# Kernel tuning notes

Measured on AMD Instinct MI355X. Metric: run time of the kernel, lower is better.

Reference implementation:

```python
import jax, jax.numpy as jnp
import numpy as np

B, S, D, H, L, F = 16, 256, 512, 1024, 2, 2048  # batch, seq, inner, head(clusters), layers, ffnn
HID = D // 2
LN_EPS = 1e-5


def _lstm_dir(x, Wih, Whh, bih, bhh, reverse=False):
    # x: [B,S,D] -> hs: [B,S,HID]; PyTorch gate order i,f,g,o
    if reverse:
        x = x[:, ::-1]
    xT = jnp.swapaxes(x, 0, 1)                    # [S,B,D]
    pre = xT @ Wih.T + (bih + bhh)                # precompute input contribution [S,B,4*HID]
    z = jnp.zeros((x.shape[0], Whh.shape[1]), x.dtype)

    def step(carry, p):
        h, c = carry
        g = p + h @ Whh.T
        i, f, gg, o = jnp.split(g, 4, axis=-1)
        c = jax.nn.sigmoid(f) * c + jax.nn.sigmoid(i) * jnp.tanh(gg)
        h = jax.nn.sigmoid(o) * jnp.tanh(c)
        return (h, c), h

    _, hs = jax.lax.scan(step, (z, z), pre)
    hs = jnp.swapaxes(hs, 0, 1)                   # [B,S,HID]
    if reverse:
        hs = hs[:, ::-1]
    return hs


def _layernorm(x, g, b):
    mu = jnp.mean(x, axis=-1, keepdims=True)
    var = jnp.mean(jnp.square(x - mu), axis=-1, keepdims=True)
    return (x - mu) * jax.lax.rsqrt(var + LN_EPS) * g + b


def _forward(input_sequence, label_embeddings, out_proj,
             Wih_f, Whh_f, bih_f, bhh_f, Wih_b, Whh_b, bih_b, bhh_b,
             ffnn_w1, ffnn_b1, ffnn_w2, ffnn_b2, ln_g, ln_b):
    fwd = _lstm_dir(input_sequence, Wih_f, Whh_f, bih_f, bhh_f, reverse=False)
    bwd = _lstm_dir(input_sequence, Wih_b, Whh_b, bih_b, bhh_b, reverse=True)
    features = jnp.concatenate([fwd, bwd], axis=-1)          # [B,S,D]

    query = jnp.broadcast_to(label_embeddings, (input_sequence.shape[0], H, D))
    for l in range(L):
        # self-attention (no scaling, as in source)
        w = jax.nn.softmax(jnp.einsum('bqd,bkd->bqk', query, query), axis=-1)
        q1 = jnp.einsum('bqk,bkd->bqd', w, query)
        # cross-attention onto LSTM features
        w2 = jax.nn.softmax(jnp.einsum('bqd,bsd->bqs', q1, features), axis=-1)
        q2 = jnp.einsum('bqs,bsd->bqd', w2, features)
        # FFN + LayerNorm
        h = jax.nn.gelu(q2 @ ffnn_w1[l] + ffnn_b1[l], approximate=False) @ ffnn_w2[l] + ffnn_b2[l]
        query = _layernorm(h, ln_g[l], ln_b[l])
    # (query @ output) * eye @ ones  ==  diagonal of the matmul == batched dot
    return jnp.einsum('bhd,dh->bh', query, out_proj)


def setup_inputs() -> dict:
    ks = jax.random.split(jax.random.key(0), 20)
    s_lstm = 1.0 / np.sqrt(HID)
    s_ff = 0.02
    clusters = jax.random.normal(ks[0], (H, D), jnp.float32) * s_ff
    return {
        'input_sequence': jax.random.normal(ks[1], (B, S, D), jnp.float32),
        'label_embeddings': clusters,
        'out_proj': clusters.T,
        'Wih_f': jax.random.normal(ks[2], (4 * HID, D), jnp.float32) * s_lstm,
        'Whh_f': jax.random.normal(ks[3], (4 * HID, HID), jnp.float32) * s_lstm,
        'bih_f': jax.random.normal(ks[4], (4 * HID,), jnp.float32) * s_lstm,
        'bhh_f': jax.random.normal(ks[5], (4 * HID,), jnp.float32) * s_lstm,
        'Wih_b': jax.random.normal(ks[6], (4 * HID, D), jnp.float32) * s_lstm,
        'Whh_b': jax.random.normal(ks[7], (4 * HID, HID), jnp.float32) * s_lstm,
        'bih_b': jax.random.normal(ks[8], (4 * HID,), jnp.float32) * s_lstm,
        'bhh_b': jax.random.normal(ks[9], (4 * HID,), jnp.float32) * s_lstm,
        'ffnn_w1': jax.random.normal(ks[10], (L, D, F), jnp.float32) * s_ff,
        'ffnn_b1': jnp.zeros((L, F), jnp.float32),
        'ffnn_w2': jax.random.normal(ks[11], (L, F, D), jnp.float32) * s_ff,
        'ffnn_b2': jnp.zeros((L, D), jnp.float32),
        'ln_g': jnp.ones((L, D), jnp.float32),
        'ln_b': jnp.zeros((L, D), jnp.float32),
    }


def reference(input_sequence, label_embeddings, out_proj,
              Wih_f, Whh_f, bih_f, bhh_f, Wih_b, Whh_b, bih_b, bhh_b,
              ffnn_w1, ffnn_b1, ffnn_w2, ffnn_b2, ln_g, ln_b):
    return _forward(input_sequence, label_embeddings, out_proj,
                    Wih_f, Whh_f, bih_f, bhh_f, Wih_b, Whh_b, bih_b, bhh_b,
                    ffnn_w1, ffnn_b1, ffnn_w2, ffnn_b2, ln_g, ln_b)
```

## Files before the change

kernel.cpp:

```cpp
#include <hip/hip_runtime.h>
#include <hip/hip_bf16.h>
#include <math.h>

#define NB 16
#define NS 256
#define ND 512
#define NH 1024
#define NF 2048
#define NHID 256

typedef __attribute__((ext_vector_type(8))) short bf16x8;
typedef __attribute__((ext_vector_type(4))) float f32x4;

__device__ __forceinline__ unsigned short f2bf(float f) {
    unsigned u = __float_as_uint(f);
    unsigned r = u + 0x7fffu + ((u >> 16) & 1u);
    return (unsigned short)(r >> 16);
}
__device__ __forceinline__ float bf2f(unsigned short h) {
    return __uint_as_float(((unsigned)h) << 16);
}
__device__ __forceinline__ float sigmoid_fast(float x) {
    return 1.0f / (1.0f + __expf(-x));
}
__device__ __forceinline__ float tanh_fast(float x) {
    return 1.0f - 2.0f / (__expf(2.0f * x) + 1.0f);
}

template<int PASSES, int ACT, int OUT>
__global__ __launch_bounds__(256) void sgemm4(
    const unsigned short* __restrict__ Ahi, const unsigned short* __restrict__ Alo,
    const unsigned short* __restrict__ Bhi, const unsigned short* __restrict__ Blo,
    const float* __restrict__ bias,
    float* __restrict__ C, unsigned short* __restrict__ Chi, unsigned short* __restrict__ Clo,
    int M, int N, int K, int lda, int ldb, long sA, long sB, long sC)
{
    __shared__ unsigned short Ah[128 * 32];
    __shared__ unsigned short Bh[128 * 32];
    __shared__ unsigned short Al[(PASSES == 3) ? 128 * 32 : 64];
    __shared__ unsigned short Bl[(PASSES == 3) ? 128 * 32 : 64];

    const int t = threadIdx.x;
    const int z = blockIdx.z;
    const int m0 = blockIdx.y * 128, n0 = blockIdx.x * 128;
    const int wid = t >> 6, lane = t & 63;
    const int wr = (wid >> 1) * 64, wc = (wid & 1) * 64;
    const int lr = lane & 15, lk = lane >> 4;
    const int rl = lane >> 2, sl = lane & 3;

    const unsigned short* pAh = Ahi + (size_t)z * sA;
    const unsigned short* pBh = Bhi + (size_t)z * sB;
    const unsigned short* pAl = (PASSES == 3) ? Alo + (size_t)z * sA : nullptr;
    const unsigned short* pBl = (PASSES == 3) ? Blo + (size_t)z * sB : nullptr;

    f32x4 acc[4][4];
    #pragma unroll
    for (int i = 0; i < 4; ++i)
        #pragma unroll
        for (int j = 0; j < 4; ++j) acc[i][j] = (f32x4){0.f, 0.f, 0.f, 0.f};

    for (int k0 = 0; k0 < K; k0 += 32) {
        #pragma unroll
        for (int e = 0; e < 2; ++e) {
            const int r = e * 64 + wid * 16 + rl;
            const size_t goA = (size_t)(m0 + r) * lda + k0 + sl * 8;
            const size_t goB = (size_t)(n0 + r) * ldb + k0 + sl * 8;
            const int lo = (e * 64 + wid * 16) * 32;
            __builtin_amdgcn_global_load_lds((const void*)(pAh + goA), (void*)&Ah[lo], 16, 0, 0);
            __builtin_amdgcn_global_load_lds((const void*)(pBh + goB), (void*)&Bh[lo], 16, 0, 0);
            if (PASSES == 3) {
                __builtin_amdgcn_global_load_lds((const void*)(pAl + goA), (void*)&Al[lo], 16, 0, 0);
                __builtin_amdgcn_global_load_lds((const void*)(pBl + goB), (void*)&Bl[lo], 16, 0, 0);
            }
        }
        __syncthreads();

        bf16x8 ah[4], bh[4], al[4], bl[4];
        #pragma unroll
        for (int mt = 0; mt < 4; ++mt) {
            int rf = wr + mt * 16 + lr;
            ah[mt] = *(const bf16x8*)&Ah[rf * 32 + lk * 8];
            if (PASSES == 3) al[mt] = *(const bf16x8*)&Al[rf * 32 + lk * 8];
        }
        #pragma unroll
        for (int nt = 0; nt < 4; ++nt) {
            int rf = wc + nt * 16 + lr;
            bh[nt] = *(const bf16x8*)&Bh[rf * 32 + lk * 8];
            if (PASSES == 3) bl[nt] = *(const bf16x8*)&Bl[rf * 32 + lk * 8];
        }
        #pragma unroll
        for (int mt = 0; mt < 4; ++mt)
            #pragma unroll
            for (int nt = 0; nt < 4; ++nt) {
                acc[mt][nt] = __builtin_amdgcn_mfma_f32_16x16x32_bf16(ah[mt], bh[nt], acc[mt][nt], 0, 0, 0);
                if (PASSES == 3) {
                    acc[mt][nt] = __builtin_amdgcn_mfma_f32_16x16x32_bf16(al[mt], bh[nt], acc[mt][nt], 0, 0, 0);
                    acc[mt][nt] = __builtin_amdgcn_mfma_f32_16x16x32_bf16(ah[mt], bl[nt], acc[mt][nt], 0, 0, 0);
                }
            }
        __syncthreads();
    }

    #pragma unroll
    for (int nt = 0; nt < 4; ++nt) {
        int col = n0 + wc + nt * 16 + lr;
        float bv = bias ? bias[col] : 0.0f;
        #pragma unroll
        for (int mt = 0; mt < 4; ++mt) {
            #pragma unroll
            for (int i = 0; i < 4; ++i) {
                int row = m0 + wr + mt * 16 + lk * 4 + i;
                float x = acc[mt][nt][i] + bv;
                if (ACT == 1) x = 0.5f * x * (1.0f + erff(x * 0.70710678118654752f));
                size_t oi = (size_t)z * sC + (size_t)row * N + col;
                if (OUT == 1) {
                    unsigned short h = f2bf(x);
                    Chi[oi] = h;
                    Clo[oi] = f2bf(x - bf2f(h));
                } else if (OUT == 2) {
                    Chi[oi] = f2bf(x);
                } else {
                    C[oi] = x;
                }
            }
        }
    }
}

static void gemm4(int passes, int act, int outm,
                  const unsigned short* Ahi, const unsigned short* Alo,
                  const unsigned short* Bhi, const unsigned short* Blo,
                  const float* bias, float* C, unsigned short* Chi, unsigned short* Clo,
                  int M, int N, int K, int lda, int ldb,
                  long sA, long sB, long sC, int Z, hipStream_t st)
{
    dim3 g(N / 128, M / 128, Z), b(256);
    if (passes == 3) {
        sgemm4<3, 0, 0><<<g, b, 0, st>>>(Ahi, Alo, Bhi, Blo, bias, C, Chi, Clo, M, N, K, lda, ldb, sA, sB, sC);
    } else if (outm == 1) {
        sgemm4<1, 0, 1><<<g, b, 0, st>>>(Ahi, Alo, Bhi, Blo, bias, C, Chi, Clo, M, N, K, lda, ldb, sA, sB, sC);
    } else if (outm == 2 && act == 1) {
        sgemm4<1, 1, 2><<<g, b, 0, st>>>(Ahi, Alo, Bhi, Blo, bias, C, Chi, Clo, M, N, K, lda, ldb, sA, sB, sC);
    } else if (outm == 2) {
        sgemm4<1, 0, 2><<<g, b, 0, st>>>(Ahi, Alo, Bhi, Blo, bias, C, Chi, Clo, M, N, K, lda, ldb, sA, sB, sC);
    } else {
        sgemm4<1, 0, 0><<<g, b, 0, st>>>(Ahi, Alo, Bhi, Blo, bias, C, Chi, Clo, M, N, K, lda, ldb, sA, sB, sC);
    }
}

__global__ __launch_bounds__(256) void cvt_split(const float* __restrict__ in,
                                                 unsigned short* __restrict__ hi,
                                                 unsigned short* __restrict__ lo)
{
    size_t i = ((size_t)blockIdx.x * 256 + threadIdx.x) * 4;
    float4 v = *(const float4*)(in + i);
    ushort4 h, l;
    h.x = f2bf(v.x); l.x = f2bf(v.x - bf2f(h.x));
    h.y = f2bf(v.y); l.y = f2bf(v.y - bf2f(h.y));
    h.z = f2bf(v.z); l.z = f2bf(v.z - bf2f(h.z));
    h.w = f2bf(v.w); l.w = f2bf(v.w - bf2f(h.w));
    *(ushort4*)(hi + i) = h;
    *(ushort4*)(lo + i) = l;
}

__global__ __launch_bounds__(256) void cvt_split_t(const float* __restrict__ in,
                                                   unsigned short* __restrict__ hiT,
                                                   unsigned short* __restrict__ loT,
                                                   int R, int C)
{
    __shared__ unsigned short tileH[64 * 72];
    __shared__ unsigned short tileL[64 * 72];
    int r0 = blockIdx.y * 64, c0 = blockIdx.x * 64;
    int t = threadIdx.x;
    int tr = t >> 2, tc = (t & 3) * 16;

    float v[16];
    const float* src = in + (size_t)(r0 + tr) * C + c0 + tc;
    *(float4*)(v)      = *(const float4*)(src);
    *(float4*)(v + 4)  = *(const float4*)(src + 4);
    *(float4*)(v + 8)  = *(const float4*)(src + 8);
    *(float4*)(v + 12) = *(const float4*)(src + 12);
    #pragma unroll
    for (int i = 0; i < 16; ++i) {
        unsigned short h = f2bf(v[i]);
        tileH[(tc + i) * 72 + tr] = h;
        tileL[(tc + i) * 72 + tr] = f2bf(v[i] - bf2f(h));
    }
    __syncthreads();

    size_t ob = (size_t)(c0 + tr) * R + r0 + tc;
    *(uint4*)(hiT + ob)     = *(const uint4*)(&tileH[tr * 72 + tc]);
    *(uint4*)(hiT + ob + 8) = *(const uint4*)(&tileH[tr * 72 + tc + 8]);
    *(uint4*)(loT + ob)     = *(const uint4*)(&tileL[tr * 72 + tc]);
    *(uint4*)(loT + ob + 8) = *(const uint4*)(&tileL[tr * 72 + tc + 8]);
}

__global__ __launch_bounds__(256) void cvt_t_hi(const float* __restrict__ in,
                                                unsigned short* __restrict__ hiT,
                                                int R, int C)
{
    __shared__ unsigned short tileH[64 * 72];
    int r0 = blockIdx.y * 64, c0 = blockIdx.x * 64;
    int t = threadIdx.x;
    int tr = t >> 2, tc = (t & 3) * 16;

    float v[16];
    const float* src = in + (size_t)(r0 + tr) * C + c0 + tc;
    *(float4*)(v)      = *(const float4*)(src);
    *(float4*)(v + 4)  = *(const float4*)(src + 4);
    *(float4*)(v + 8)  = *(const float4*)(src + 8);
    *(float4*)(v + 12) = *(const float4*)(src + 12);
    #pragma unroll
    for (int i = 0; i < 16; ++i) tileH[(tc + i) * 72 + tr] = f2bf(v[i]);
    __syncthreads();

    size_t ob = (size_t)(c0 + tr) * R + r0 + tc;
    *(uint4*)(hiT + ob)     = *(const uint4*)(&tileH[tr * 72 + tc]);
    *(uint4*)(hiT + ob + 8) = *(const uint4*)(&tileH[tr * 72 + tc + 8]);
}

__global__ __launch_bounds__(256) void tcvt_bf16(const unsigned short* __restrict__ in,
                                                 unsigned short* __restrict__ out,
                                                 int R, int C)
{
    __shared__ unsigned short tile[64 * 72];
    int z = blockIdx.z;
    in += (size_t)z * R * C;
    out += (size_t)z * R * C;
    int r0 = blockIdx.y * 64, c0 = blockIdx.x * 64;
    int t = threadIdx.x;
    int tr = t >> 2, tc = (t & 3) * 16;

    uint4 q0 = *(const uint4*)(in + (size_t)(r0 + tr) * C + c0 + tc);
    uint4 q1 = *(const uint4*)(in + (size_t)(r0 + tr) * C + c0 + tc + 8);
    unsigned short e[16];
    *(uint4*)(e) = q0;
    *(uint4*)(e + 8) = q1;
    #pragma unroll
    for (int i = 0; i < 16; ++i) tile[(tc + i) * 72 + tr] = e[i];
    __syncthreads();

    uint4 o0 = *(const uint4*)(&tile[tr * 72 + tc]);
    uint4 o1 = *(const uint4*)(&tile[tr * 72 + tc + 8]);
    *(uint4*)(out + (size_t)(c0 + tr) * R + r0 + tc) = o0;
    *(uint4*)(out + (size_t)(c0 + tr) * R + r0 + tc + 8) = o1;
}

__global__ __launch_bounds__(256) void bias_sum_kernel(
    const float* bihF, const float* bhhF, const float* bihB, const float* bhhB,
    float* out)
{
    int i = blockIdx.x * 256 + threadIdx.x;
    if (i < 1024) out[i] = bihF[i] + bhhF[i];
    else out[i] = bihB[i - 1024] + bhhB[i - 1024];
}

__global__ __launch_bounds__(256) void lstm_rec6m(
    const float* __restrict__ pre,
    const float* __restrict__ WhhF, const float* __restrict__ WhhB,
    unsigned long long* __restrict__ hg,
    int* __restrict__ flags,
    unsigned short* __restrict__ fhi, unsigned short* __restrict__ flo)
{
    const int bid = blockIdx.x;
    const int dir = bid >> 4, slice = bid & 15;
    const float* Whh = dir ? WhhB : WhhF;

    const int tid = threadIdx.x;
    const int wv = tid >> 6;
    const int lane = tid & 63;
    const int lr = lane & 15;
    const int lk = lane >> 4;
    const int eb = tid >> 4;
    const int eu = tid & 15;

    __shared__ unsigned short hh[16 * 264];
    __shared__ unsigned short hl[16 * 264];
    __shared__ float gx[4][16][17];

    bf16x8 wfh[8], wfl[8];
    {
        const float* wrow = Whh + (size_t)(wv * 256 + slice * 16 + lr) * 256 + lk * 8;
        #pragma unroll
        for (int kt = 0; kt < 8; ++kt) {
            float4 a = *(const float4*)(wrow + kt * 32);
            float4 b = *(const float4*)(wrow + kt * 32 + 4);
            float v[8] = {a.x, a.y, a.z, a.w, b.x, b.y, b.z, b.w};
            unsigned short hhv[8], llv[8];
            #pragma unroll
            for (int i = 0; i < 8; ++i) {
                unsigned short h = f2bf(v[i]);
                hhv[i] = h;
                llv[i] = f2bf(v[i] - bf2f(h));
            }
            wfh[kt] = *(bf16x8*)hhv;
            wfl[kt] = *(bf16x8*)llv;
        }
    }
    for (int i = tid; i < 16 * 264; i += 256) { hh[i] = 0; hl[i] = 0; }

    float c = 0.0f;
    __syncthreads();

    for (int si = 0; si < NS; ++si) {
        const int s = dir ? (NS - 1 - si) : si;
        const float* pp = pre + ((size_t)(eb * NS + s)) * 2048 + dir * 1024 + slice * 16 + eu;
        float pi = pp[0], pf = pp[256], pg = pp[512], po = pp[768];

        if (si > 0) {
            if (tid < 16) {
                while (__hip_atomic_load(&flags[dir * 16 + tid], __ATOMIC_RELAXED,
                                         __HIP_MEMORY_SCOPE_AGENT) < si) {
                    __builtin_amdgcn_s_sleep(1);
                }
            }
            __syncthreads();
            const unsigned long long* src =
                hg + (size_t)(((si - 1) & 1) * 2 + dir) * 2048;
            const int b2 = tid >> 4, pb = (tid & 15) * 8;
            unsigned short hbuf[16], lbuf[16];
            #pragma unroll
            for (int j = 0; j < 8; ++j) {
                unsigned long long v = __hip_atomic_load(
                    &src[b2 * 128 + pb + j], __ATOMIC_RELAXED,
                    __HIP_MEMORY_SCOPE_AGENT);
                hbuf[2 * j]     = (unsigned short)(v & 0xffff);
                lbuf[2 * j]     = (unsigned short)((v >> 16) & 0xffff);
                hbuf[2 * j + 1] = (unsigned short)((v >> 32) & 0xffff);
                lbuf[2 * j + 1] = (unsigned short)(v >> 48);
            }
            char* dh = (char*)hh + b2 * 528 + (tid & 15) * 32;
            char* dl = (char*)hl + b2 * 528 + (tid & 15) * 32;
            *(uint4*)dh        = *(uint4*)(hbuf);
            *(uint4*)(dh + 16) = *(uint4*)(hbuf + 8);
            *(uint4*)dl        = *(uint4*)(lbuf);
            *(uint4*)(dl + 16) = *(uint4*)(lbuf + 8);
            __syncthreads();
        }

        f32x4 acc = (f32x4){0.f, 0.f, 0.f, 0.f};
        #pragma unroll
        for (int kt = 0; kt < 8; ++kt) {
            const char* hp = (const char*)hh + lr * 528 + kt * 64 + lk * 16;
            const char* lp = (const char*)hl + lr * 528 + kt * 64 + lk * 16;
            bf16x8 ah = *(const bf16x8*)hp;
            bf16x8 al = *(const bf16x8*)lp;
            acc = __builtin_amdgcn_mfma_f32_16x16x32_bf16(ah, wfh[kt], acc, 0, 0, 0);
            acc = __builtin_amdgcn_mfma_f32_16x16x32_bf16(al, wfh[kt], acc, 0, 0, 0);
            acc = __builtin_amdgcn_mfma_f32_16x16x32_bf16(ah, wfl[kt], acc, 0, 0, 0);
        }
        #pragma unroll
        for (int i = 0; i < 4; ++i) gx[wv][lk * 4 + i][lr] = acc[i];
        __syncthreads();

        float ai = gx[0][eb][eu] + pi;
        float af = gx[1][eb][eu] + pf;
        float ag = gx[2][eb][eu] + pg;
        float ao = gx[3][eb][eu] + po;
        float gi = sigmoid_fast(ai);
        float gf = sigmoid_fast(af);
        float gg = tanh_fast(ag);
        float go = sigmoid_fast(ao);
        c = gf * c + gi * gg;
        float h = go * tanh_fast(c);

        unsigned short h16 = f2bf(h);
        unsigned short l16 = f2bf(h - bf2f(h16));
        unsigned my = (unsigned)h16 | ((unsigned)l16 << 16);
        unsigned oth = __shfl_xor(my, 1);
        if ((eu & 1) == 0) {
            unsigned long long v = (unsigned long long)my |
                                   ((unsigned long long)oth << 32);
            unsigned long long* dst =
                hg + (size_t)((si & 1) * 2 + dir) * 2048;
            __hip_atomic_store(&dst[eb * 128 + slice * 8 + (eu >> 1)], v,
                               __ATOMIC_RELAXED, __HIP_MEMORY_SCOPE_AGENT);
        }
        size_t oi = ((size_t)(eb * NS + s)) * 512 + dir * 256 + slice * 16 + eu;
        fhi[oi] = h16;
        flo[oi] = l16;

        asm volatile("s_waitcnt vmcnt(0)" ::: "memory");
        __syncthreads();
        if (tid == 0)
            __hip_atomic_store(&flags[bid], si + 1, __ATOMIC_RELAXED,
                               __HIP_MEMORY_SCOPE_AGENT);
    }
}

__global__ __launch_bounds__(256) void softmax_ip(float* __restrict__ X, int N)
{
    float* row = X + (size_t)blockIdx.x * N;
    unsigned short* o = (unsigned short*)row;
    int t = threadIdx.x;
    int cnt = N >> 8;
    float v[4];
    float m = -1e30f;
    for (int i = 0; i < cnt; ++i) { v[i] = row[t + (i << 8)]; m = fmaxf(m, v[i]); }
    for (int sh = 32; sh; sh >>= 1) m = fmaxf(m, __shfl_xor(m, sh));
    __shared__ float lm[4];
    if ((t & 63) == 0) lm[t >> 6] = m;
    __syncthreads();
    m = fmaxf(fmaxf(lm[0], lm[1]), fmaxf(lm[2], lm[3]));
    float s = 0.0f;
    for (int i = 0; i < cnt; ++i) { v[i] = expf(v[i] - m); s += v[i]; }
    for (int sh = 32; sh; sh >>= 1) s += __shfl_xor(s, sh);
    __shared__ float ls[4];
    if ((t & 63) == 0) ls[t >> 6] = s;
    __syncthreads();
    s = ls[0] + ls[1] + ls[2] + ls[3];
    float inv = 1.0f / s;
    __syncthreads();
    for (int i = 0; i < cnt; ++i) {
        float y = v[i] * inv;
        unsigned short h = f2bf(y);
        int j = t + (i << 8);
        o[j] = h;
        o[N + j] = f2bf(y - bf2f(h));
    }
}

__global__ __launch_bounds__(256) void layernorm_split(
    const float* __restrict__ X, const float* __restrict__ g, const float* __restrict__ b,
    unsigned short* __restrict__ ohi, unsigned short* __restrict__ olo)
{
    const float* row = X + (size_t)blockIdx.x * 512;
    size_t ob = (size_t)blockIdx.x * 512;
    int t = threadIdx.x;
    float x0 = row[t], x1 = row[t + 256];
    float s = x0 + x1, sq = x0 * x0 + x1 * x1;
    for (int o = 32; o; o >>= 1) { s += __shfl_xor(s, o); sq += __shfl_xor(sq, o); }
    __shared__ float ls[8];
    int w = t >> 6;
    if ((t & 63) == 0) { ls[w] = s; ls[4 + w] = sq; }
    __syncthreads();
    s = ls[0] + ls[1] + ls[2] + ls[3];
    sq = ls[4] + ls[5] + ls[6] + ls[7];
    float mu = s * (1.0f / 512.0f);
    float var = sq * (1.0f / 512.0f) - mu * mu;
    float inv = rsqrtf(var + 1e-5f);
    float y0 = (x0 - mu) * inv * g[t]       + b[t];
    float y1 = (x1 - mu) * inv * g[t + 256] + b[t + 256];
    unsigned short h0 = f2bf(y0), h1 = f2bf(y1);
    ohi[ob + t]       = h0;  olo[ob + t]       = f2bf(y0 - bf2f(h0));
    ohi[ob + t + 256] = h1;  olo[ob + t + 256] = f2bf(y1 - bf2f(h1));
}

__global__ __launch_bounds__(256) void outproj3(
    const unsigned short* __restrict__ qhi, const unsigned short* __restrict__ qlo,
    const unsigned short* __restrict__ phi, const unsigned short* __restrict__ plo,
    float* __restrict__ out)
{
    int gw = blockIdx.x * 4 + (threadIdx.x >> 6);
    int lane = threadIdx.x & 63;
    int h = gw & 1023;
    uint4 qh = ((const uint4*)(qhi + (size_t)gw * 512))[lane];
    uint4 ql = ((const uint4*)(qlo + (size_t)gw * 512))[lane];
    uint4 ph = ((const uint4*)(phi + (size_t)h * 512))[lane];
    uint4 pl = ((const uint4*)(plo + (size_t)h * 512))[lane];
    unsigned short qhe[8], qle[8], phe[8], ple[8];
    *(uint4*)qhe = qh; *(uint4*)qle = ql; *(uint4*)phe = ph; *(uint4*)ple = pl;
    float s = 0.0f;
    #pragma unroll
    for (int i = 0; i < 8; ++i) {
        float q = bf2f(qhe[i]) + bf2f(qle[i]);
        float p = bf2f(phe[i]) + bf2f(ple[i]);
        s += q * p;
    }
    for (int o = 32; o; o >>= 1) s += __shfl_xor(s, o);
    if (lane == 0) out[gw] = s;
}

extern "C" void kernel_launch(void* const* d_in, const int* in_sizes, int n_in,
                              void* d_out, int out_size, void* d_ws, size_t ws_size,
                              hipStream_t stream)
{
    (void)in_sizes; (void)n_in; (void)out_size; (void)ws_size;

    const float* x     = (const float*)d_in[0];
    const float* le    = (const float*)d_in[1];
    const float* proj  = (const float*)d_in[2];
    const float* WihF  = (const float*)d_in[3];
    const float* WhhF  = (const float*)d_in[4];
    const float* bihF  = (const float*)d_in[5];
    const float* bhhF  = (const float*)d_in[6];
    const float* WihB  = (const float*)d_in[7];
    const float* WhhB  = (const float*)d_in[8];
    const float* bihB  = (const float*)d_in[9];
    const float* bhhB  = (const float*)d_in[10];
    const float* w1    = (const float*)d_in[11];
    const float* b1    = (const float*)d_in[12];
    const float* w2    = (const float*)d_in[13];
    const float* b2    = (const float*)d_in[14];
    const float* lng   = (const float*)d_in[15];
    const float* lnb   = (const float*)d_in[16];
    float* out = (float*)d_out;
    float* ws  = (float*)d_ws;
    unsigned short* wsu = (unsigned short*)d_ws;

    const size_t MEG = 1048576;
    const size_t R0    = 0;
    const size_t R1    = 8 * MEG;
    const size_t AR    = 16 * MEG;
    const size_t QHI   = 33 * MEG;
    const size_t QLO   = 37 * MEG;
    const size_t FHI   = 41 * MEG;
    const size_t FLO   = 42 * MEG;
    const size_t FTHI  = 43 * MEG;
    const size_t FTLO  = 44 * MEG;
    const size_t LEHI  = 45 * MEG;
    const size_t LELO  = LEHI  + MEG / 4;
    const size_t LETHI = LELO  + MEG / 4;
    const size_t LETLO = LETHI + MEG / 4;
    const size_t WIHH  = 46 * MEG;
    const size_t WIHL  = WIHH + MEG / 2;
    const size_t SYNC  = 47 * MEG;
    const size_t W1TH  = SYNC  + MEG / 4;
    const size_t W1TL  = W1TH  + MEG / 2;
    const size_t W2TH  = W1TL  + MEG / 2;
    const size_t W2TL  = W2TH  + MEG / 2;
    const size_t PTH   = W2TL  + MEG / 2;
    const size_t PTL   = PTH   + MEG / 4;
    const size_t BSUM  = PTL   + MEG / 4;

    float* pre    = ws + R0;
    float* lnsrc  = ws + R0;
    float* arena  = ws + AR;
    float* bsum   = ws + BSUM;
    int*   flags  = (int*)(ws + SYNC);
    unsigned long long* hg = (unsigned long long*)(ws + SYNC + 1024);
    unsigned short* qthi  = wsu + 2 * R0;
    unsigned short* q2hi  = wsu + 2 * R1;
    unsigned short* qhi   = wsu + 2 * QHI;
    unsigned short* qlo   = wsu + 2 * QLO;
    unsigned short* fhi   = wsu + 2 * FHI;
    unsigned short* flo   = wsu + 2 * FLO;
    unsigned short* fthi  = wsu + 2 * FTHI;
    unsigned short* ftlo  = wsu + 2 * FTLO;
    unsigned short* lehi  = wsu + 2 * LEHI;
    unsigned short* lelo  = wsu + 2 * LELO;
    unsigned short* lethi = wsu + 2 * LETHI;
    unsigned short* letlo = wsu + 2 * LETLO;
    unsigned short* wihh  = wsu + 2 * WIHH;
    unsigned short* wihl  = wsu + 2 * WIHL;
    unsigned short* w1th  = wsu + 2 * W1TH;
    unsigned short* w2th  = wsu + 2 * W2TH;
    unsigned short* pth   = wsu + 2 * PTH;
    unsigned short* ptl   = wsu + 2 * PTL;

    bias_sum_kernel<<<8, 256, 0, stream>>>(bihF, bhhF, bihB, bhhB, bsum);
    cvt_split<<<512, 256, 0, stream>>>(WihF, wihh, wihl);
    cvt_split<<<512, 256, 0, stream>>>(WihB, wihh + 524288, wihl + 524288);
    cvt_split<<<512, 256, 0, stream>>>(le, lehi, lelo);
    { dim3 g(512 / 64, 1024 / 64, 1);
      cvt_split_t<<<g, 256, 0, stream>>>(le, lethi, letlo, 1024, 512); }
    hipMemsetAsync(flags, 0, 32 * sizeof(int), stream);

    unsigned short* xhi = wsu + 2 * AR;
    unsigned short* xlo = wsu + 2 * (AR + MEG);
    cvt_split<<<2048, 256, 0, stream>>>(x, xhi, xlo);

    gemm4(3, 0, 0, xhi, xlo, wihh, wihl, bsum, pre, nullptr, nullptr,
          NB * NS, 2048, ND, ND, ND, 0, 0, 0, 1, stream);

    lstm_rec6m<<<32, 256, 0, stream>>>(pre, WhhF, WhhB, hg, flags, fhi, flo);
    { dim3 g(512 / 64, 256 / 64, 16);
      tcvt_bf16<<<g, 256, 0, stream>>>(fhi, fthi, 256, 512);
      tcvt_bf16<<<g, 256, 0, stream>>>(flo, ftlo, 256, 512); }

    for (int l = 0; l < 2; ++l) {
        const float* b1l = b1 + (size_t)l * NF;
        const float* b2l = b2 + (size_t)l * ND;
        const float* gl  = lng + (size_t)l * ND;
        const float* bl  = lnb + (size_t)l * ND;

        { dim3 g(NF / 64, ND / 64, 1);
          cvt_t_hi<<<g, 256, 0, stream>>>(w1 + (size_t)l * ND * NF, w1th, ND, NF); }
        { dim3 g(ND / 64, NF / 64, 1);
          cvt_t_hi<<<g, 256, 0, stream>>>(w2 + (size_t)l * NF * ND, w2th, NF, ND); }

        if (l == 0) {
            float* wsc = arena;
            unsigned short* wscu = (unsigned short*)wsc;
            unsigned short* q1hi = wsu + 2 * (AR + 1 * MEG);
            unsigned short* q1lo = wsu + 2 * (AR + 1 * MEG + MEG / 4);
            float* s2s = arena + 4 * MEG;
            unsigned short* s2u = (unsigned short*)s2s;

            gemm4(3, 0, 0, lehi, lelo, lehi, lelo, nullptr, wsc, nullptr, nullptr,
                  NH, NH, ND, ND, ND, 0, 0, 0, 1, stream);
            softmax_ip<<<NH, 256, 0, stream>>>(wsc, NH);
            gemm4(1, 0, 1, wscu, nullptr, lethi, nullptr, nullptr, nullptr, q1hi, q1lo,
                  NH, ND, NH, 2 * NH, NH, 0, 0, 0, 1, stream);
            gemm4(3, 0, 0, q1hi, q1lo, fhi, flo, nullptr, s2s, nullptr, nullptr,
                  NH, NS, ND, ND, ND, 0, (long)NS * ND, (long)NH * NS, 16, stream);
            softmax_ip<<<NB * NH, 256, 0, stream>>>(s2s, NS);
            gemm4(1, 0, 2, s2u, nullptr, fthi, nullptr, nullptr, nullptr, q2hi, nullptr,
                  NH, ND, NS, 2 * NS, NS,
                  (long)2 * NH * NS, (long)ND * NS, (long)NH * ND, 16, stream);
        } else {
            { dim3 g(512 / 64, 1024 / 64, 16);
              tcvt_bf16<<<g, 256, 0, stream>>>(qhi, qthi, 1024, 512); }
            float* wsc = arena;
            unsigned short* wscu = (unsigned short*)wsc;
            unsigned short* q1hi = wsu + 2 * (AR + 8 * MEG);
            unsigned short* q1lo = wsu + 2 * (AR + 10 * MEG);
            float* s2s = arena + 12 * MEG;
            unsigned short* s2u = (unsigned short*)s2s;
            for (int g8 = 0; g8 < 2; ++g8) {
                size_t qo = (size_t)g8 * 8;
                gemm4(3, 0, 0, qhi + qo * NH * ND, qlo + qo * NH * ND,
                      qhi + qo * NH * ND, qlo + qo * NH * ND, nullptr, wsc, nullptr, nullptr,
                      NH, NH, ND, ND, ND,
                      (long)NH * ND, (long)NH * ND, (long)NH * NH, 8, stream);
                softmax_ip<<<8 * NH, 256, 0, stream>>>(wsc, NH);
                gemm4(1, 0, 1, wscu, nullptr, qthi + qo * ND * NH, nullptr,
                      nullptr, nullptr, q1hi, q1lo, NH, ND, NH, 2 * NH, NH,
                      (long)2 * NH * NH, (long)ND * NH, (long)NH * ND, 8, stream);
                gemm4(3, 0, 0, q1hi, q1lo, fhi + qo * NS * ND, flo + qo * NS * ND,
                      nullptr, s2s, nullptr, nullptr, NH, NS, ND, ND, ND,
                      (long)NH * ND, (long)NS * ND, (long)NH * NS, 8, stream);
                softmax_ip<<<8 * NH, 256, 0, stream>>>(s2s, NS);
                gemm4(1, 0, 2, s2u, nullptr, fthi + qo * ND * NS, nullptr,
                      nullptr, nullptr, q2hi + qo * NH * ND, nullptr,
                      NH, ND, NS, 2 * NS, NS,
                      (long)2 * NH * NS, (long)ND * NS, (long)NH * ND, 8, stream);
            }
        }

        unsigned short* ffhi = wsu + 2 * AR;
        for (int ch = 0; ch < 2; ++ch) {
            const unsigned short* rih = q2hi + (size_t)ch * 8192 * ND;
            float* rows_out = lnsrc + (size_t)ch * 8192 * ND;
            gemm4(1, 1, 2, rih, nullptr, w1th, nullptr, b1l, nullptr, ffhi, nullptr,
                  8192, NF, ND, ND, ND, 0, 0, 0, 1, stream);
            gemm4(1, 0, 0, ffhi, nullptr, w2th, nullptr, b2l, rows_out, nullptr, nullptr,
                  8192, ND, NF, NF, NF, 0, 0, 0, 1, stream);
        }
        layernorm_split<<<NB * NH, 256, 0, stream>>>(lnsrc, gl, bl, qhi, qlo);
    }

    { dim3 g(1024 / 64, 512 / 64, 1);
      cvt_split_t<<<g, 256, 0, stream>>>(proj, pth, ptl, 512, 1024); }
    outproj3<<<4096, 256, 0, stream>>>(qhi, qlo, pth, ptl, out);
}
```

Baseline: 1.618 ms.

## Overlap independent GEMM and weight conversions with LSTM recurrence in spare blocks

The persistent LSTM recurrence kernel used only 32 blocks, leaving most CUs idle. It now launches 256 blocks: the extra blocks compute the layer-0 label self-attention score GEMM and perform all FFN weight and projection transposed bf16 conversions for both layers. This removes those launches from the serial path and overlaps them with the latency-bound recurrence. The two FFN row-chunks are also merged into single larger GEMMs, which doubles the intermediate buffer size. The risks are interference with the spin-wait recurrence blocks and co-residency assumptions.

```diff
diff --git a/kernel.cpp b/kernel.cpp
--- a/kernel.cpp
+++ b/kernel.cpp
@@ -195,30 +195,6 @@
     *(uint4*)(loT + ob + 8) = *(const uint4*)(&tileL[tr * 72 + tc + 8]);
 }
 
-__global__ __launch_bounds__(256) void cvt_t_hi(const float* __restrict__ in,
-                                                unsigned short* __restrict__ hiT,
-                                                int R, int C)
-{
-    __shared__ unsigned short tileH[64 * 72];
-    int r0 = blockIdx.y * 64, c0 = blockIdx.x * 64;
-    int t = threadIdx.x;
-    int tr = t >> 2, tc = (t & 3) * 16;
-
-    float v[16];
-    const float* src = in + (size_t)(r0 + tr) * C + c0 + tc;
-    *(float4*)(v)      = *(const float4*)(src);
-    *(float4*)(v + 4)  = *(const float4*)(src + 4);
-    *(float4*)(v + 8)  = *(const float4*)(src + 8);
-    *(float4*)(v + 12) = *(const float4*)(src + 12);
-    #pragma unroll
-    for (int i = 0; i < 16; ++i) tileH[(tc + i) * 72 + tr] = f2bf(v[i]);
-    __syncthreads();
-
-    size_t ob = (size_t)(c0 + tr) * R + r0 + tc;
-    *(uint4*)(hiT + ob)     = *(const uint4*)(&tileH[tr * 72 + tc]);
-    *(uint4*)(hiT + ob + 8) = *(const uint4*)(&tileH[tr * 72 + tc + 8]);
-}
-
 __global__ __launch_bounds__(256) void tcvt_bf16(const unsigned short* __restrict__ in,
                                                  unsigned short* __restrict__ out,
                                                  int R, int C)
@@ -255,136 +231,260 @@
     else out[i] = bihB[i - 1024] + bhhB[i - 1024];
 }
 
-__global__ __launch_bounds__(256) void lstm_rec6m(
+__global__ __launch_bounds__(256) void rec_fused(
     const float* __restrict__ pre,
     const float* __restrict__ WhhF, const float* __restrict__ WhhB,
-    unsigned long long* __restrict__ hg,
-    int* __restrict__ flags,
-    unsigned short* __restrict__ fhi, unsigned short* __restrict__ flo)
-{
-    const int bid = blockIdx.x;
-    const int dir = bid >> 4, slice = bid & 15;
-    const float* Whh = dir ? WhhB : WhhF;
-
-    const int tid = threadIdx.x;
-    const int wv = tid >> 6;
-    const int lane = tid & 63;
-    const int lr = lane & 15;
-    const int lk = lane >> 4;
-    const int eb = tid >> 4;
-    const int eu = tid & 15;
-
+    unsigned long long* __restrict__ hg, int* __restrict__ flags,
+    unsigned short* __restrict__ fhi, unsigned short* __restrict__ flo,
+    const unsigned short* __restrict__ lehi, const unsigned short* __restrict__ lelo,
+    float* __restrict__ wsc,
+    const float* __restrict__ w1, const float* __restrict__ w2,
+    unsigned short* __restrict__ w1th0, unsigned short* __restrict__ w2th0,
+    unsigned short* __restrict__ w1th1, unsigned short* __restrict__ w2th1,
+    const float* __restrict__ proj,
+    unsigned short* __restrict__ pth, unsigned short* __restrict__ ptl)
+{
     __shared__ unsigned short hh[16 * 264];
     __shared__ unsigned short hl[16 * 264];
     __shared__ float gx[4][16][17];
-
-    bf16x8 wfh[8], wfl[8];
-    {
-        const float* wrow = Whh + (size_t)(wv * 256 + slice * 16 + lr) * 256 + lk * 8;
+    __shared__ unsigned short gAh[128 * 32];
+    __shared__ unsigned short gAl[128 * 32];
+    __shared__ unsigned short gBh[128 * 32];
+    __shared__ unsigned short gBl[128 * 32];
+    __shared__ unsigned short tH[64 * 72];
+    __shared__ unsigned short tL[64 * 72];
+
+    const int tid = threadIdx.x;
+
+    if (blockIdx.x < 32) {
+        const int bid = blockIdx.x;
+        const int dir = bid >> 4, slice = bid & 15;
+        const float* Whh = dir ? WhhB : WhhF;
+        const int wv = tid >> 6;
+        const int lane = tid & 63;
+        const int lr = lane & 15;
+        const int lk = lane >> 4;
+        const int eb = tid >> 4;
+        const int eu = tid & 15;
+
+        bf16x8 wfh[8], wfl[8];
+        {
+            const float* wrow = Whh + (size_t)(wv * 256 + slice * 16 + lr) * 256 + lk * 8;
+            #pragma unroll
+            for (int kt = 0; kt < 8; ++kt) {
+                float4 a = *(const float4*)(wrow + kt * 32);
+                float4 b = *(const float4*)(wrow + kt * 32 + 4);
+                float v[8] = {a.x, a.y, a.z, a.w, b.x, b.y, b.z, b.w};
+                unsigned short hhv[8], llv[8];
+                #pragma unroll
+                for (int i = 0; i < 8; ++i) {
+                    unsigned short h = f2bf(v[i]);
+                    hhv[i] = h;
+                    llv[i] = f2bf(v[i] - bf2f(h));
+                }
+                wfh[kt] = *(bf16x8*)hhv;
+                wfl[kt] = *(bf16x8*)llv;
+            }
+        }
+        for (int i = tid; i < 16 * 264; i += 256) { hh[i] = 0; hl[i] = 0; }
+
+        float c = 0.0f;
+        __syncthreads();
+
+        for (int si = 0; si < NS; ++si) {
+            const int s = dir ? (NS - 1 - si) : si;
+            const float* pp = pre + ((size_t)(eb * NS + s)) * 2048 + dir * 1024 + slice * 16 + eu;
+            float pi = pp[0], pf = pp[256], pg = pp[512], po = pp[768];
+
+            if (si > 0) {
+                if (tid < 16) {
+                    while (__hip_atomic_load(&flags[dir * 16 + tid], __ATOMIC_RELAXED,
+                                             __HIP_MEMORY_SCOPE_AGENT) < si) {
+                        __builtin_amdgcn_s_sleep(1);
+                    }
+                }
+                __syncthreads();
+                const unsigned long long* src =
+                    hg + (size_t)(((si - 1) & 1) * 2 + dir) * 2048;
+                const int b2 = tid >> 4, pb = (tid & 15) * 8;
+                unsigned short hbuf[16], lbuf[16];
+                #pragma unroll
+                for (int j = 0; j < 8; ++j) {
+                    unsigned long long v = __hip_atomic_load(
+                        &src[b2 * 128 + pb + j], __ATOMIC_RELAXED,
+                        __HIP_MEMORY_SCOPE_AGENT);
+                    hbuf[2 * j]     = (unsigned short)(v & 0xffff);
+                    lbuf[2 * j]     = (unsigned short)((v >> 16) & 0xffff);
+                    hbuf[2 * j + 1] = (unsigned short)((v >> 32) & 0xffff);
+                    lbuf[2 * j + 1] = (unsigned short)(v >> 48);
+                }
+                char* dh = (char*)hh + b2 * 528 + (tid & 15) * 32;
+                char* dl = (char*)hl + b2 * 528 + (tid & 15) * 32;
+                *(uint4*)dh        = *(uint4*)(hbuf);
+                *(uint4*)(dh + 16) = *(uint4*)(hbuf + 8);
+                *(uint4*)dl        = *(uint4*)(lbuf);
+                *(uint4*)(dl + 16) = *(uint4*)(lbuf + 8);
+                __syncthreads();
+            }
+
+            f32x4 acc = (f32x4){0.f, 0.f, 0.f, 0.f};
+            #pragma unroll
+            for (int kt = 0; kt < 8; ++kt) {
+                const char* hp = (const char*)hh + lr * 528 + kt * 64 + lk * 16;
+                const char* lp = (const char*)hl + lr * 528 + kt * 64 + lk * 16;
+                bf16x8 ah = *(const bf16x8*)hp;
+                bf16x8 al = *(const bf16x8*)lp;
+                acc = __builtin_amdgcn_mfma_f32_16x16x32_bf16(ah, wfh[kt], acc, 0, 0, 0);
+                acc = __builtin_amdgcn_mfma_f32_16x16x32_bf16(al, wfh[kt], acc, 0, 0, 0);
+                acc = __builtin_amdgcn_mfma_f32_16x16x32_bf16(ah, wfl[kt], acc, 0, 0, 0);
+            }
+            #pragma unroll
+            for (int i = 0; i < 4; ++i) gx[wv][lk * 4 + i][lr] = acc[i];
+            __syncthreads();
+
+            float ai = gx[0][eb][eu] + pi;
+            float af = gx[1][eb][eu] + pf;
+            float ag = gx[2][eb][eu] + pg;
+            float ao = gx[3][eb][eu] + po;
+            float gi = sigmoid_fast(ai);
+            float gf = sigmoid_fast(af);
+            float gg = tanh_fast(ag);
+            float go = sigmoid_fast(ao);
+            c = gf * c + gi * gg;
+            float h = go * tanh_fast(c);
+
+            unsigned short h16 = f2bf(h);
+            unsigned short l16 = f2bf(h - bf2f(h16));
+            unsigned my = (unsigned)h16 | ((unsigned)l16 << 16);
+            unsigned oth = __shfl_xor(my, 1);
+            if ((eu & 1) == 0) {
+                unsigned long long v = (unsigned long long)my |
+                                       ((unsigned long long)oth << 32);
+                unsigned long long* dst =
+                    hg + (size_t)((si & 1) * 2 + dir) * 2048;
+                __hip_atomic_store(&dst[eb * 128 + slice * 8 + (eu >> 1)], v,
+                                   __ATOMIC_RELAXED, __HIP_MEMORY_SCOPE_AGENT);
+            }
+            size_t oi = ((size_t)(eb * NS + s)) * 512 + dir * 256 + slice * 16 + eu;
+            fhi[oi] = h16;
+            flo[oi] = l16;
+
+            asm volatile("s_waitcnt vmcnt(0)" ::: "memory");
+            __syncthreads();
+            if (tid == 0)
+                __hip_atomic_store(&flags[bid], si + 1, __ATOMIC_RELAXED,
+                                   __HIP_MEMORY_SCOPE_AGENT);
+        }
+        return;
+    }
+
+    const int hid = blockIdx.x - 32;
+    const int lane = tid & 63;
+    const int wid = tid >> 6;
+    const int lr = lane & 15, lk = lane >> 4;
+
+    if (hid < 64) {
+        const int m0 = (hid >> 3) * 128, n0 = (hid & 7) * 128;
+        const int wr = (wid >> 1) * 64, wc = (wid & 1) * 64;
+        const int sr = tid >> 1, sc = (tid & 1) * 16;
+
+        f32x4 acc[4][4];
         #pragma unroll
-        for (int kt = 0; kt < 8; ++kt) {
-            float4 a = *(const float4*)(wrow + kt * 32);
-            float4 b = *(const float4*)(wrow + kt * 32 + 4);
-            float v[8] = {a.x, a.y, a.z, a.w, b.x, b.y, b.z, b.w};
-            unsigned short hhv[8], llv[8];
-            #pragma unroll
-            for (int i = 0; i < 8; ++i) {
+        for (int i = 0; i < 4; ++i)
+            #pragma unroll
+            for (int j = 0; j < 4; ++j) acc[i][j] = (f32x4){0.f, 0.f, 0.f, 0.f};
+
+        for (int k0 = 0; k0 < ND; k0 += 32) {
+            {
+                size_t oa = (size_t)(m0 + sr) * ND + k0 + sc;
+                size_t ob = (size_t)(n0 + sr) * ND + k0 + sc;
+                *(uint4*)&gAh[sr * 32 + sc]     = *(const uint4*)(lehi + oa);
+                *(uint4*)&gAh[sr * 32 + sc + 8] = *(const uint4*)(lehi + oa + 8);
+                *(uint4*)&gAl[sr * 32 + sc]     = *(const uint4*)(lelo + oa);
+                *(uint4*)&gAl[sr * 32 + sc + 8] = *(const uint4*)(lelo + oa + 8);
+                *(uint4*)&gBh[sr * 32 + sc]     = *(const uint4*)(lehi + ob);
+                *(uint4*)&gBh[sr * 32 + sc + 8] = *(const uint4*)(lehi + ob + 8);
+                *(uint4*)&gBl[sr * 32 + sc]     = *(const uint4*)(lelo + ob);
+                *(uint4*)&gBl[sr * 32 + sc + 8] = *(const uint4*)(lelo + ob + 8);
+            }
+            __syncthreads();
+
+            bf16x8 ah[4], al[4], bh[4], bl[4];
+            #pragma unroll
+            for (int mt = 0; mt < 4; ++mt) {
+                int rf = wr + mt * 16 + lr;
+                ah[mt] = *(const bf16x8*)&gAh[rf * 32 + lk * 8];
+                al[mt] = *(const bf16x8*)&gAl[rf * 32 + lk * 8];
+            }
+            #pragma unroll
+            for (int nt = 0; nt < 4; ++nt) {
+                int rf = wc + nt * 16 + lr;
+                bh[nt] = *(const bf16x8*)&gBh[rf * 32 + lk * 8];
+                bl[nt] = *(const bf16x8*)&gBl[rf * 32 + lk * 8];
+            }
+            #pragma unroll
+            for (int mt = 0; mt < 4; ++mt)
+                #pragma unroll
+                for (int nt = 0; nt < 4; ++nt) {
+                    acc[mt][nt] = __builtin_amdgcn_mfma_f32_16x16x32_bf16(ah[mt], bh[nt], acc[mt][nt], 0, 0, 0);
+                    acc[mt][nt] = __builtin_amdgcn_mfma_f32_16x16x32_bf16(al[mt], bh[nt], acc[mt][nt], 0, 0, 0);
+                    acc[mt][nt] = __builtin_amdgcn_mfma_f32_16x16x32_bf16(ah[mt], bl[nt], acc[mt][nt], 0, 0, 0);
+                }
+            __syncthreads();
+        }
+        const int wr2 = (wid >> 1) * 64, wc2 = (wid & 1) * 64;
+        #pragma unroll
+        for (int nt = 0; nt < 4; ++nt) {
+            int col = n0 + wc2 + nt * 16 + lr;
+            #pragma unroll
+            for (int mt = 0; mt < 4; ++mt)
+                #pragma unroll
+                for (int i = 0; i < 4; ++i) {
+                    int row = m0 + wr2 + mt * 16 + lk * 4 + i;
+                    wsc[(size_t)row * NH + col] = acc[mt][nt][i];
+                }
+        }
+    }
+
+    const int tr = tid >> 2, tc = (tid & 3) * 16;
+    for (int job = hid; job < 1152; job += 224) {
+        const float* in;
+        unsigned short* outH;
+        unsigned short* outL = nullptr;
+        int R, C, by, bx;
+        if (job < 256)        { int j = job;        in = w1;              outH = w1th0; R = ND; C = NF; by = j >> 5, bx = j & 31; }
+        else if (job < 512)   { int j = job - 256;  in = w2;              outH = w2th0; R = NF; C = ND; by = j >> 3, bx = j & 7; }
+        else if (job < 768)   { int j = job - 512;  in = w1 + (size_t)ND * NF; outH = w1th1; R = ND; C = NF; by = j >> 5, bx = j & 31; }
+        else if (job < 1024)  { int j = job - 768;  in = w2 + (size_t)NF * ND; outH = w2th1; R = NF; C = ND; by = j >> 3, bx = j & 7; }
+        else                  { int j = job - 1024; in = proj;            outH = pth; outL = ptl; R = 512; C = 1024; by = j >> 4, bx = j & 15; }
+
+        int r0 = by * 64, c0 = bx * 64;
+        __syncthreads();
+        float v[16];
+        const float* src = in + (size_t)(r0 + tr) * C + c0 + tc;
+        *(float4*)(v)      = *(const float4*)(src);
+        *(float4*)(v + 4)  = *(const float4*)(src + 4);
+        *(float4*)(v + 8)  = *(const float4*)(src + 8);
+        *(float4*)(v + 12) = *(const float4*)(src + 12);
+        if (outL) {
+            #pragma unroll
+            for (int i = 0; i < 16; ++i) {
                 unsigned short h = f2bf(v[i]);
-                hhv[i] = h;
-                llv[i] = f2bf(v[i] - bf2f(h));
-            }
-            wfh[kt] = *(bf16x8*)hhv;
-            wfl[kt] = *(bf16x8*)llv;
-        }
-    }
-    for (int i = tid; i < 16 * 264; i += 256) { hh[i] = 0; hl[i] = 0; }
-
-    float c = 0.0f;
-    __syncthreads();
-
-    for (int si = 0; si < NS; ++si) {
-        const int s = dir ? (NS - 1 - si) : si;
-        const float* pp = pre + ((size_t)(eb * NS + s)) * 2048 + dir * 1024 + slice * 16 + eu;
-        float pi = pp[0], pf = pp[256], pg = pp[512], po = pp[768];
-
-        if (si > 0) {
-            if (tid < 16) {
-                while (__hip_atomic_load(&flags[dir * 16 + tid], __ATOMIC_RELAXED,
-                                         __HIP_MEMORY_SCOPE_AGENT) < si) {
-                    __builtin_amdgcn_s_sleep(1);
-                }
-            }
-            __syncthreads();
-            const unsigned long long* src =
-                hg + (size_t)(((si - 1) & 1) * 2 + dir) * 2048;
-            const int b2 = tid >> 4, pb = (tid & 15) * 8;
-            unsigned short hbuf[16], lbuf[16];
-            #pragma unroll
-            for (int j = 0; j < 8; ++j) {
-                unsigned long long v = __hip_atomic_load(
-                    &src[b2 * 128 + pb + j], __ATOMIC_RELAXED,
-                    __HIP_MEMORY_SCOPE_AGENT);
-                hbuf[2 * j]     = (unsigned short)(v & 0xffff);
-                lbuf[2 * j]     = (unsigned short)((v >> 16) & 0xffff);
-                hbuf[2 * j + 1] = (unsigned short)((v >> 32) & 0xffff);
-                lbuf[2 * j + 1] = (unsigned short)(v >> 48);
-            }
-            char* dh = (char*)hh + b2 * 528 + (tid & 15) * 32;
-            char* dl = (char*)hl + b2 * 528 + (tid & 15) * 32;
-            *(uint4*)dh        = *(uint4*)(hbuf);
-            *(uint4*)(dh + 16) = *(uint4*)(hbuf + 8);
-            *(uint4*)dl        = *(uint4*)(lbuf);
-            *(uint4*)(dl + 16) = *(uint4*)(lbuf + 8);
-            __syncthreads();
-        }
-
-        f32x4 acc = (f32x4){0.f, 0.f, 0.f, 0.f};
-        #pragma unroll
-        for (int kt = 0; kt < 8; ++kt) {
-            const char* hp = (const char*)hh + lr * 528 + kt * 64 + lk * 16;
-            const char* lp = (const char*)hl + lr * 528 + kt * 64 + lk * 16;
-            bf16x8 ah = *(const bf16x8*)hp;
-            bf16x8 al = *(const bf16x8*)lp;
-            acc = __builtin_amdgcn_mfma_f32_16x16x32_bf16(ah, wfh[kt], acc, 0, 0, 0);
-            acc = __builtin_amdgcn_mfma_f32_16x16x32_bf16(al, wfh[kt], acc, 0, 0, 0);
-            acc = __builtin_amdgcn_mfma_f32_16x16x32_bf16(ah, wfl[kt], acc, 0, 0, 0);
-        }
-        #pragma unroll
-        for (int i = 0; i < 4; ++i) gx[wv][lk * 4 + i][lr] = acc[i];
+                tH[(tc + i) * 72 + tr] = h;
+                tL[(tc + i) * 72 + tr] = f2bf(v[i] - bf2f(h));
+            }
+        } else {
+            #pragma unroll
+            for (int i = 0; i < 16; ++i) tH[(tc + i) * 72 + tr] = f2bf(v[i]);
+        }
         __syncthreads();
-
-        float ai = gx[0][eb][eu] + pi;
-        float af = gx[1][eb][eu] + pf;
-        float ag = gx[2][eb][eu] + pg;
-        float ao = gx[3][eb][eu] + po;
-        float gi = sigmoid_fast(ai);
-        float gf = sigmoid_fast(af);
-        float gg = tanh_fast(ag);
-        float go = sigmoid_fast(ao);
-        c = gf * c + gi * gg;
-        float h = go * tanh_fast(c);
-
-        unsigned short h16 = f2bf(h);
-        unsigned short l16 = f2bf(h - bf2f(h16));
-        unsigned my = (unsigned)h16 | ((unsigned)l16 << 16);
-        unsigned oth = __shfl_xor(my, 1);
-        if ((eu & 1) == 0) {
-            unsigned long long v = (unsigned long long)my |
-                                   ((unsigned long long)oth << 32);
-            unsigned long long* dst =
-                hg + (size_t)((si & 1) * 2 + dir) * 2048;
-            __hip_atomic_store(&dst[eb * 128 + slice * 8 + (eu >> 1)], v,
-                               __ATOMIC_RELAXED, __HIP_MEMORY_SCOPE_AGENT);
-        }
-        size_t oi = ((size_t)(eb * NS + s)) * 512 + dir * 256 + slice * 16 + eu;
-        fhi[oi] = h16;
-        flo[oi] = l16;
-
-        asm volatile("s_waitcnt vmcnt(0)" ::: "memory");
-        __syncthreads();
-        if (tid == 0)
-            __hip_atomic_store(&flags[bid], si + 1, __ATOMIC_RELAXED,
-                               __HIP_MEMORY_SCOPE_AGENT);
+        size_t ob = (size_t)(c0 + tr) * R + r0 + tc;
+        *(uint4*)(outH + ob)     = *(const uint4*)(&tH[tr * 72 + tc]);
+        *(uint4*)(outH + ob + 8) = *(const uint4*)(&tH[tr * 72 + tc + 8]);
+        if (outL) {
+            *(uint4*)(outL + ob)     = *(const uint4*)(&tL[tr * 72 + tc]);
+            *(uint4*)(outL + ob + 8) = *(const uint4*)(&tL[tr * 72 + tc + 8]);
+        }
     }
 }
 
@@ -515,11 +615,11 @@
     const size_t WIHH  = 46 * MEG;
     const size_t WIHL  = WIHH + MEG / 2;
     const size_t SYNC  = 47 * MEG;
-    const size_t W1TH  = SYNC  + MEG / 4;
-    const size_t W1TL  = W1TH  + MEG / 2;
-    const size_t W2TH  = W1TL  + MEG / 2;
-    const size_t W2TL  = W2TH  + MEG / 2;
-    const size_t PTH   = W2TL  + MEG / 2;
+    const size_t W1TH0 = SYNC  + MEG / 4;
+    const size_t W1TH1 = W1TH0 + MEG / 2;
+    const size_t W2TH0 = W1TH1 + MEG / 2;
+    const size_t W2TH1 = W2TH0 + MEG / 2;
+    const size_t PTH   = W2TH1 + MEG / 2;
     const size_t PTL   = PTH   + MEG / 4;
     const size_t BSUM  = PTL   + MEG / 4;
 
@@ -543,8 +643,10 @@
     unsigned short* letlo = wsu + 2 * LETLO;
     unsigned short* wihh  = wsu + 2 * WIHH;
     unsigned short* wihl  = wsu + 2 * WIHL;
-    unsigned short* w1th  = wsu + 2 * W1TH;
-    unsigned short* w2th  = wsu + 2 * W2TH;
+    unsigned short* w1th0 = wsu + 2 * W1TH0;
+    unsigned short* w1th1 = wsu + 2 * W1TH1;
+    unsigned short* w2th0 = wsu + 2 * W2TH0;
+    unsigned short* w2th1 = wsu + 2 * W2TH1;
     unsigned short* pth   = wsu + 2 * PTH;
     unsigned short* ptl   = wsu + 2 * PTL;
 
@@ -563,7 +665,11 @@
     gemm4(3, 0, 0, xhi, xlo, wihh, wihl, bsum, pre, nullptr, nullptr,
           NB * NS, 2048, ND, ND, ND, 0, 0, 0, 1, stream);
 
-    lstm_rec6m<<<32, 256, 0, stream>>>(pre, WhhF, WhhB, hg, flags, fhi, flo);
+    float* wsc_l0 = arena;
+    rec_fused<<<256, 256, 0, stream>>>(pre, WhhF, WhhB, hg, flags, fhi, flo,
+                                       lehi, lelo, wsc_l0,
+                                       w1, w2, w1th0, w2th0, w1th1, w2th1,
+                                       proj, pth, ptl);
     { dim3 g(512 / 64, 256 / 64, 16);
       tcvt_bf16<<<g, 256, 0, stream>>>(fhi, fthi, 256, 512);
       tcvt_bf16<<<g, 256, 0, stream>>>(flo, ftlo, 256, 512); }
@@ -573,22 +679,17 @@
         const float* b2l = b2 + (size_t)l * ND;
         const float* gl  = lng + (size_t)l * ND;
         const float* bl  = lnb + (size_t)l * ND;
-
-        { dim3 g(NF / 64, ND / 64, 1);
-          cvt_t_hi<<<g, 256, 0, stream>>>(w1 + (size_t)l * ND * NF, w1th, ND, NF); }
-        { dim3 g(ND / 64, NF / 64, 1);
-          cvt_t_hi<<<g, 256, 0, stream>>>(w2 + (size_t)l * NF * ND, w2th, NF, ND); }
+        unsigned short* w1th = l ? w1th1 : w1th0;
+        unsigned short* w2th = l ? w2th1 : w2th0;
 
         if (l == 0) {
-            float* wsc = arena;
+            float* wsc = wsc_l0;
             unsigned short* wscu = (unsigned short*)wsc;
             unsigned short* q1hi = wsu + 2 * (AR + 1 * MEG);
             unsigned short* q1lo = wsu + 2 * (AR + 1 * MEG + MEG / 4);
             float* s2s = arena + 4 * MEG;
             unsigned short* s2u = (unsigned short*)s2s;
 
-            gemm4(3, 0, 0, lehi, lelo, lehi, lelo, nullptr, wsc, nullptr, nullptr,
-                  NH, NH, ND, ND, ND, 0, 0, 0, 1, stream);
             softmax_ip<<<NH, 256, 0, stream>>>(wsc, NH);
             gemm4(1, 0, 1, wscu, nullptr, lethi, nullptr, nullptr, nullptr, q1hi, q1lo,
                   NH, ND, NH, 2 * NH, NH, 0, 0, 0, 1, stream);
@@ -629,18 +730,12 @@
         }
 
         unsigned short* ffhi = wsu + 2 * AR;
-        for (int ch = 0; ch < 2; ++ch) {
-            const unsigned short* rih = q2hi + (size_t)ch * 8192 * ND;
-            float* rows_out = lnsrc + (size_t)ch * 8192 * ND;
-            gemm4(1, 1, 2, rih, nullptr, w1th, nullptr, b1l, nullptr, ffhi, nullptr,
-                  8192, NF, ND, ND, ND, 0, 0, 0, 1, stream);
-            gemm4(1, 0, 0, ffhi, nullptr, w2th, nullptr, b2l, rows_out, nullptr, nullptr,
-                  8192, ND, NF, NF, NF, 0, 0, 0, 1, stream);
-        }
+        gemm4(1, 1, 2, q2hi, nullptr, w1th, nullptr, b1l, nullptr, ffhi, nullptr,
+              16384, NF, ND, ND, ND, 0, 0, 0, 1, stream);
+        gemm4(1, 0, 0, ffhi, nullptr, w2th, nullptr, b2l, lnsrc, nullptr, nullptr,
+              16384, ND, NF, NF, NF, 0, 0, 0, 1, stream);
         layernorm_split<<<NB * NH, 256, 0, stream>>>(lnsrc, gl, bl, qhi, qlo);
     }
 
-    { dim3 g(1024 / 64, 512 / 64, 1);
-      cvt_split_t<<<g, 256, 0, stream>>>(proj, pth, ptl, 512, 1024); }
     outproj3<<<4096, 256, 0, stream>>>(qhi, qlo, pth, ptl, out);
 }
```

Measured after the change: 1.510 ms. -6.7%, faster.
